# Performance work log

Measured on AMD Instinct MI355X. Metric: run time of the kernel, lower is better.

The kernel has to match this reference:

```python
import jax, jax.numpy as jnp
import numpy as np

CHUNK = 1000  # CHUNK_SIZE in the torch source
H = 8         # num_heads


def _depthwise_chunked(x_t, Wl, bl):
    """Replicates torch per-chunk local_conv (depthwise k=3, pad=1) + residual.
    Zero padding occurs at every chunk boundary, exactly as in the source loop.
    x_t: [B, C, L] with L divisible by CHUNK. Wl: [C,1,3], bl: [C].
    """
    B, C, L = x_t.shape
    n = L // CHUNK
    xc = x_t.reshape(B, C, n, CHUNK).transpose(0, 2, 1, 3).reshape(B * n, C, CHUNK)
    y = jax.lax.conv_general_dilated(
        xc, Wl, window_strides=(1,), padding=((1, 1),),
        feature_group_count=C, dimension_numbers=('NCH', 'OIH', 'NCH'))
    y = y + bl[None, :, None] + xc  # conv bias + residual (kv_chunk = local_conv(kv_chunk) + kv_chunk)
    return y.reshape(B, n, C, CHUNK).transpose(0, 2, 1, 3).reshape(B, C, L)


def setup_inputs() -> dict:
    key = jax.random.key(0)
    ks = jax.random.split(key, 8)
    B, L, C = 4, 2000, 512
    x = jax.random.normal(ks[0], (B, L, C), dtype=jnp.float32)
    rpe = jax.random.normal(ks[1], (1, H, L, L), dtype=jnp.float32) * 0.02
    s = 1.0 / np.sqrt(C)
    Wq = jax.random.normal(ks[2], (C, C), dtype=jnp.float32) * s      # q: Conv1d(dim,dim,1)
    bq = jnp.zeros((C,), dtype=jnp.float32)
    Wkv = jax.random.normal(ks[3], (2 * C, C), dtype=jnp.float32) * s # kv: Conv1d(dim,2dim,1)
    bkv = jnp.zeros((2 * C,), dtype=jnp.float32)
    Wl = jax.random.normal(ks[4], (C, 1, 3), dtype=jnp.float32) * (1.0 / np.sqrt(3.0))  # depthwise k=3
    bl = jnp.zeros((C,), dtype=jnp.float32)
    return {"x": x, "relative_pos_enc": rpe, "Wq": Wq, "bq": bq,
            "Wkv": Wkv, "bkv": bkv, "Wl": Wl, "bl": bl}


def reference(x, relative_pos_enc, Wq, bq, Wkv, bkv, Wl, bl):
    B, L, C = x.shape
    hd = C // H
    scale = hd ** (-0.5)
    x_t = jnp.swapaxes(x, 1, 2)  # [B, C, L]
    # q projection (1x1 conv == linear over channels)
    q = jnp.einsum('oc,bcl->bol', Wq, x_t) + bq[None, :, None]
    q = q.reshape(B, H, hd, L).transpose(0, 1, 3, 2)  # [B, H, L, hd]
    # K/V path: sr = Identity (sr_ratio=1); chunked depthwise local conv + residual
    kv_in = _depthwise_chunked(x_t, Wl, bl)           # [B, C, L]
    kv = jnp.einsum('oc,bcl->bol', Wkv, kv_in) + bkv[None, :, None]  # [B, 2C, L]
    k = kv[:, :C].reshape(B, H, hd, L)                # [B, H, hd, L]
    v = kv[:, C:].reshape(B, H, hd, L).transpose(0, 1, 3, 2)  # [B, H, L, hd]
    # attention with additive relative-position bias (chunking over rows in the
    # source is math-equivalent since softmax rows are independent)
    attn = jnp.einsum('bhld,bhdm->bhlm', q, k) * scale + relative_pos_enc
    attn = jax.nn.softmax(attn, axis=-1)
    out = jnp.einsum('bhlm,bhmd->bhld', attn, v)      # [B, H, L, hd]
    # source: cat -> [B,H,L,hd] -> transpose(-1,-2) -> [B,H,hd,L] -> reshape(B,L,C)
    return out.transpose(0, 1, 3, 2).reshape(B, L, C)
```

## Files before the change

### kernel.cpp

```cpp
#include <hip/hip_runtime.h>

#define B_ 4
#define L_ 2000
#define LP 2048
#define C_ 512
#define H_ 8
#define HD 64
#define CHUNK_ 1000

typedef __attribute__((ext_vector_type(8))) short bf16x8;
typedef __attribute__((ext_vector_type(4))) float f32x4;

__device__ inline unsigned short f2bf(float f) {
    union { float f; unsigned int u; } v; v.f = f;
    unsigned int r = v.u + 0x7fffu + ((v.u >> 16) & 1u);
    return (unsigned short)(r >> 16);
}

__global__ void conv_kernel(const float* __restrict__ x, const float* __restrict__ Wl,
                            const float* __restrict__ bl,
                            unsigned short* __restrict__ kv16,
                            unsigned short* __restrict__ x16) {
    int i4 = blockIdx.x * 256 + threadIdx.x;
    if (i4 >= B_ * L_ * C_ / 4) return;
    int idx = i4 * 4;
    int c = idx & (C_ - 1);
    int l = (idx >> 9) % L_;
    int p = l % CHUNK_;
    float4 xc = *(const float4*)&x[idx];
    float4 lf = (p > 0)          ? *(const float4*)&x[idx - C_] : make_float4(0, 0, 0, 0);
    float4 rt = (p < CHUNK_ - 1) ? *(const float4*)&x[idx + C_] : make_float4(0, 0, 0, 0);
    float y[4];
    const float* xcp = &xc.x; const float* lfp = &lf.x; const float* rtp = &rt.x;
#pragma unroll
    for (int j = 0; j < 4; j++) {
        y[j] = xcp[j] + bl[c + j] + Wl[(c + j) * 3 + 0] * lfp[j]
             + Wl[(c + j) * 3 + 1] * xcp[j] + Wl[(c + j) * 3 + 2] * rtp[j];
    }
    ushort4 kv = make_ushort4(f2bf(y[0]), f2bf(y[1]), f2bf(y[2]), f2bf(y[3]));
    ushort4 xo = make_ushort4(f2bf(xcp[0]), f2bf(xcp[1]), f2bf(xcp[2]), f2bf(xcp[3]));
    *(ushort4*)&kv16[idx] = kv;
    *(ushort4*)&x16[idx]  = xo;
}

__global__ void cvt_kernel(const float* __restrict__ Wq, const float* __restrict__ Wkv,
                           unsigned short* __restrict__ Wq16,
                           unsigned short* __restrict__ Wkv16) {
    int i4 = blockIdx.x * 256 + threadIdx.x;
    int idx = i4 * 4;
    const float* src; unsigned short* dst; int off;
    if (idx < 262144) { src = Wq; dst = Wq16; off = idx; }
    else if (idx < 786432) { src = Wkv; dst = Wkv16; off = idx - 262144; }
    else return;
    float4 v = *(const float4*)&src[off];
    *(ushort4*)&dst[off] = make_ushort4(f2bf(v.x), f2bf(v.y), f2bf(v.z), f2bf(v.w));
}

__global__ __launch_bounds__(256) void proj_mfma(
    const unsigned short* __restrict__ A, const unsigned short* __restrict__ W,
    const float* __restrict__ bias,
    unsigned short* __restrict__ o0, unsigned short* __restrict__ o1, int mode) {
    __shared__ __align__(16) unsigned short tile[64][72];
    const int tid = threadIdx.x;
    const int lane = tid & 63;
    const int wave = tid >> 6;
    const int c = lane & 15;
    const int quad = lane >> 4;
    const int mrow = blockIdx.x * 64 + wave * 16 + c;
    const int n0 = blockIdx.y * 64;
    f32x4 acc[4] = {{0,0,0,0},{0,0,0,0},{0,0,0,0},{0,0,0,0}};
    const unsigned short* Ap = A + (size_t)mrow * C_ + quad * 8;
#pragma unroll 4
    for (int k0 = 0; k0 < C_; k0 += 32) {
        bf16x8 a = *(const bf16x8*)(Ap + k0);
#pragma unroll
        for (int t = 0; t < 4; t++) {
            bf16x8 wv = *(const bf16x8*)&W[(size_t)(n0 + 16 * t + c) * C_ + k0 + quad * 8];
            acc[t] = __builtin_amdgcn_mfma_f32_16x16x32_bf16(a, wv, acc[t], 0, 0, 0);
        }
    }
    const bool vpath = (mode == 1 && n0 >= C_);
    const int lm = wave * 16 + quad * 4;
#pragma unroll
    for (int t = 0; t < 4; t++) {
        float bv = bias[n0 + 16 * t + c];
#pragma unroll
        for (int r = 0; r < 4; r++) {
            unsigned short val = f2bf(acc[t][r] + bv);
            if (!vpath) tile[lm + r][16 * t + c] = val;
            else        tile[16 * t + c][lm + r] = val;
        }
    }
    __syncthreads();
    if (!vpath) {
        int lr = tid >> 2, chunk = (tid & 3) * 16;
        int m = blockIdx.x * 64 + lr;
        int b = m / L_, l = m % L_;
        int nn = (n0 + chunk) & (C_ - 1);
        int h = nn >> 6, d0 = nn & 63;
        unsigned short* dst = &o0[(((size_t)(b * H_ + h) * LP) + l) * HD + d0];
        *(uint4*)dst       = *(const uint4*)&tile[lr][chunk];
        *(uint4*)(dst + 8) = *(const uint4*)&tile[lr][chunk + 8];
    } else {
        int dr = tid >> 2, chunk = (tid & 3) * 16;
        int nn = (n0 - C_) + dr;
        int h = nn >> 6, d = nn & 63;
        int mbase = blockIdx.x * 64 + chunk;
        int b0 = mbase / L_, b1 = (mbase + 15) / L_;
        if (b0 == b1) {
            int l = mbase % L_;
            unsigned short* dst = &o1[(((size_t)(b0 * H_ + h) * HD) + d) * LP + l];
            *(uint4*)dst       = *(const uint4*)&tile[dr][chunk];
            *(uint4*)(dst + 8) = *(const uint4*)&tile[dr][chunk + 8];
        } else {
            for (int i = 0; i < 16; i++) {
                int m = mbase + i;
                int b = m / L_, l = m % L_;
                o1[(((size_t)(b * H_ + h) * HD) + d) * LP + l] = tile[dr][chunk + i];
            }
        }
    }
}

__global__ __launch_bounds__(256, 2) void attn_mfma(
    const unsigned short* __restrict__ Q, const unsigned short* __restrict__ K,
    const unsigned short* __restrict__ Vt, const float* __restrict__ rpe,
    float* __restrict__ po, float* __restrict__ lsum) {
    __shared__ __align__(16) unsigned short Ks[4][32][72];
    __shared__ __align__(16) unsigned short Vs[4][64][40];
    __shared__ __align__(16) unsigned short Ps[4][2][16][40];
    const int tid = threadIdx.x;
    const int lane = tid & 63;
    const int wave = tid >> 6;
    const int c = lane & 15;
    const int quad = lane >> 4;
    const int bid = blockIdx.x;
    const int ks = bid & 1;
    const int h  = (bid >> 1) & 7;
    const int rt = bid >> 4;
    const int r0w = rt * 64 + wave * 16;
    const int rg0 = r0w + quad * 4;
    const int rgc = min(r0w + c, L_ - 1);
    const float* rrow = rpe + (size_t)h * L_ * L_ + (size_t)rgc * L_;

    const int krow = tid >> 3, kcol = (tid & 7) * 8;
    const int vrow = tid >> 2, vcol = (tid & 3) * 8;

    const int kt0 = ks * 32, kt1 = kt0 + 32;

    const unsigned short* Kb0 = K + (size_t)(0 * H_ + h) * LP * HD
        + (size_t)krow * HD + kcol + (size_t)(kt0 * 32) * HD;
    const unsigned short* Kb1 = Kb0 + (size_t)H_ * LP * HD;
    const unsigned short* Kb2 = Kb1 + (size_t)H_ * LP * HD;
    const unsigned short* Kb3 = Kb2 + (size_t)H_ * LP * HD;
    const unsigned short* Vb0 = Vt + (size_t)(0 * H_ + h) * HD * LP
        + (size_t)vrow * LP + vcol + kt0 * 32;
    const unsigned short* Vb1 = Vb0 + (size_t)H_ * HD * LP;
    const unsigned short* Vb2 = Vb1 + (size_t)H_ * HD * LP;
    const unsigned short* Vb3 = Vb2 + (size_t)H_ * HD * LP;

    bf16x8 qf0[4], qf1[4];
#pragma unroll
    for (int b = 0; b < 4; b++) {
        const unsigned short* Qb = Q + (size_t)(b * H_ + h) * LP * HD;
        qf0[b] = *(const bf16x8*)&Qb[(size_t)(r0w + c) * HD + quad * 8];
        qf1[b] = *(const bf16x8*)&Qb[(size_t)(r0w + c) * HD + 32 + quad * 8];
    }

    float l_i[4] = {0.f, 0.f, 0.f, 0.f};
    f32x4 o_acc[4][4];
#pragma unroll
    for (int b = 0; b < 4; b++)
#pragma unroll
        for (int t = 0; t < 4; t++) o_acc[b][t] = (f32x4){0.f, 0.f, 0.f, 0.f};

    const float LOG2E = 1.44269504f;
#define LOAD_RPE(d0, d1, KT)                                                 \
    {                                                                        \
        int cb0 = (KT) * 32 + quad * 4;                                      \
        int cb1 = cb0 + 16;                                                  \
        float4 raw0 = *(const float4*)&rrow[min(cb0, L_ - 4)];               \
        float4 raw1 = *(const float4*)&rrow[min(cb1, L_ - 4)];               \
        d0 = (cb0 <= L_ - 4) ? make_float4(raw0.x * LOG2E, raw0.y * LOG2E,   \
                                           raw0.z * LOG2E, raw0.w * LOG2E)  \
                             : make_float4(-1e30f, -1e30f, -1e30f, -1e30f);  \
        d1 = (cb1 <= L_ - 4) ? make_float4(raw1.x * LOG2E, raw1.y * LOG2E,   \
                                           raw1.z * LOG2E, raw1.w * LOG2E)  \
                             : make_float4(-1e30f, -1e30f, -1e30f, -1e30f);  \
    }

    uint4 kpre0 = *(const uint4*)Kb0, kpre1 = *(const uint4*)Kb1;
    uint4 kpre2 = *(const uint4*)Kb2, kpre3 = *(const uint4*)Kb3;
    uint4 vpre0 = *(const uint4*)Vb0, vpre1 = *(const uint4*)Vb1;
    uint4 vpre2 = *(const uint4*)Vb2, vpre3 = *(const uint4*)Vb3;
    float4 rpl0, rpl1;
    LOAD_RPE(rpl0, rpl1, kt0)

    for (int kt = kt0; kt < kt1; kt++) {
        __syncthreads();
        *(uint4*)&Ks[0][krow][kcol] = kpre0;
        *(uint4*)&Ks[1][krow][kcol] = kpre1;
        *(uint4*)&Ks[2][krow][kcol] = kpre2;
        *(uint4*)&Ks[3][krow][kcol] = kpre3;
        *(uint4*)&Vs[0][vrow][vcol] = vpre0;
        *(uint4*)&Vs[1][vrow][vcol] = vpre1;
        *(uint4*)&Vs[2][vrow][vcol] = vpre2;
        *(uint4*)&Vs[3][vrow][vcol] = vpre3;
        __syncthreads();

        float4 rpn0, rpn1;
        if (kt + 1 < kt1) {
            const size_t ko = (size_t)(kt + 1 - kt0) * 32 * HD;
            const int    vo = (kt + 1 - kt0) * 32;
            kpre0 = *(const uint4*)(Kb0 + ko);
            kpre1 = *(const uint4*)(Kb1 + ko);
            kpre2 = *(const uint4*)(Kb2 + ko);
            kpre3 = *(const uint4*)(Kb3 + ko);
            vpre0 = *(const uint4*)(Vb0 + vo);
            vpre1 = *(const uint4*)(Vb1 + vo);
            vpre2 = *(const uint4*)(Vb2 + vo);
            vpre3 = *(const uint4*)(Vb3 + vo);
            LOAD_RPE(rpn0, rpn1, kt + 1)
        }

#pragma unroll
        for (int b = 0; b < 4; b++) {
            f32x4 s0, s1;
            {
                bf16x8 k0f = *(const bf16x8*)&Ks[b][c][quad * 8];
                bf16x8 k1f = *(const bf16x8*)&Ks[b][c][32 + quad * 8];
                f32x4 z = {0.f, 0.f, 0.f, 0.f};
                z = __builtin_amdgcn_mfma_f32_16x16x32_bf16(k0f, qf0[b], z, 0, 0, 0);
                s0 = __builtin_amdgcn_mfma_f32_16x16x32_bf16(k1f, qf1[b], z, 0, 0, 0);
            }
            {
                bf16x8 k0f = *(const bf16x8*)&Ks[b][16 + c][quad * 8];
                bf16x8 k1f = *(const bf16x8*)&Ks[b][16 + c][32 + quad * 8];
                f32x4 z = {0.f, 0.f, 0.f, 0.f};
                z = __builtin_amdgcn_mfma_f32_16x16x32_bf16(k0f, qf0[b], z, 0, 0, 0);
                s1 = __builtin_amdgcn_mfma_f32_16x16x32_bf16(k1f, qf1[b], z, 0, 0, 0);
            }
            float psum;
            {
                float p0 = exp2f(fmaf(s0[0], 0.18033688f, rpl0.x));
                float p1 = exp2f(fmaf(s0[1], 0.18033688f, rpl0.y));
                float p2 = exp2f(fmaf(s0[2], 0.18033688f, rpl0.z));
                float p3 = exp2f(fmaf(s0[3], 0.18033688f, rpl0.w));
                psum = (p0 + p1) + (p2 + p3);
                *(ushort4*)&Ps[wave][b & 1][c][quad * 4] =
                    make_ushort4(f2bf(p0), f2bf(p1), f2bf(p2), f2bf(p3));
            }
            {
                float p0 = exp2f(fmaf(s1[0], 0.18033688f, rpl1.x));
                float p1 = exp2f(fmaf(s1[1], 0.18033688f, rpl1.y));
                float p2 = exp2f(fmaf(s1[2], 0.18033688f, rpl1.z));
                float p3 = exp2f(fmaf(s1[3], 0.18033688f, rpl1.w));
                psum += (p0 + p1) + (p2 + p3);
                *(ushort4*)&Ps[wave][b & 1][c][16 + quad * 4] =
                    make_ushort4(f2bf(p0), f2bf(p1), f2bf(p2), f2bf(p3));
            }
            l_i[b] += psum;
            bf16x8 pa = *(const bf16x8*)&Ps[wave][b & 1][c][quad * 8];
#pragma unroll
            for (int t = 0; t < 4; t++) {
                bf16x8 v0 = *(const bf16x8*)&Vs[b][16 * t + c][quad * 8];
                o_acc[b][t] = __builtin_amdgcn_mfma_f32_16x16x32_bf16(pa, v0, o_acc[b][t], 0, 0, 0);
            }
        }
        if (kt + 1 < kt1) { rpl0 = rpn0; rpl1 = rpn1; }
    }

#pragma unroll
    for (int b = 0; b < 4; b++) {
        float v = l_i[b];
        v += __shfl_xor(v, 16);
        v += __shfl_xor(v, 32);
        float* pob = po + (size_t)(ks * 32 + b * H_ + h) * L_ * HD;
#pragma unroll
        for (int t = 0; t < 4; t++) {
            int d = 16 * t + c;
#pragma unroll
            for (int r = 0; r < 4; r++) {
                int l = rg0 + r;
                if (l < L_) pob[(size_t)l * HD + d] = o_acc[b][t][r];
            }
        }
        if (lane < 16) {
            float* lb = lsum + (size_t)(ks * 32 + b * H_ + h) * LP;
            lb[r0w + lane] = v;
        }
    }
#undef LOAD_RPE
}

__global__ __launch_bounds__(256) void merge_kernel(
    const float* __restrict__ po, const float* __restrict__ lsum,
    float* __restrict__ out) {
    __shared__ __align__(16) float T[64][68];
    const int tid = threadIdx.x;
    const int bh = blockIdx.x >> 5;
    const int lt = blockIdx.x & 31;
    const float* p0 = po + (size_t)bh * L_ * HD;
    const float* p1 = p0 + (size_t)32 * L_ * HD;
    const float* ls0 = lsum + (size_t)bh * LP;
    const float* ls1 = ls0 + (size_t)32 * LP;
#pragma unroll
    for (int it = 0; it < 4; it++) {
        int idx = it * 256 + tid;
        int row = idx >> 4;
        int dc = (idx & 15) * 4;
        int l = lt * 64 + row;
        float4 v = make_float4(0.f, 0.f, 0.f, 0.f);
        if (l < L_) {
            float4 a  = *(const float4*)&p0[(size_t)l * HD + dc];
            float4 b4 = *(const float4*)&p1[(size_t)l * HD + dc];
            float inv = 1.f / (ls0[l] + ls1[l]);
            v = make_float4((a.x + b4.x) * inv, (a.y + b4.y) * inv,
                            (a.z + b4.z) * inv, (a.w + b4.w) * inv);
        }
        T[dc + 0][row] = v.x; T[dc + 1][row] = v.y;
        T[dc + 2][row] = v.z; T[dc + 3][row] = v.w;
    }
    __syncthreads();
    const int d = tid >> 2, ch = (tid & 3) * 16;
    const int lbase = lt * 64 + ch;
    if (lbase + 15 < L_) {
        float* dst = &out[((size_t)(bh * HD + d)) * L_ + lbase];
#pragma unroll
        for (int i = 0; i < 4; i++)
            *(float4*)&dst[4 * i] = *(const float4*)&T[d][ch + 4 * i];
    }
}

extern "C" void kernel_launch(void* const* d_in, const int* in_sizes, int n_in,
                              void* d_out, int out_size, void* d_ws, size_t ws_size,
                              hipStream_t stream) {
    const float* x   = (const float*)d_in[0];
    const float* rpe = (const float*)d_in[1];
    const float* Wq  = (const float*)d_in[2];
    const float* bq  = (const float*)d_in[3];
    const float* Wkv = (const float*)d_in[4];
    const float* bkv = (const float*)d_in[5];
    const float* Wl  = (const float*)d_in[6];
    const float* bl  = (const float*)d_in[7];
    float* out = (float*)d_out;

    unsigned short* wsu  = (unsigned short*)d_ws;
    unsigned short* x16  = wsu;
    unsigned short* kv16 = wsu + 4096000;
    unsigned short* Wq16 = wsu + 8192000;
    unsigned short* Wkv16= wsu + 8454144;
    unsigned short* Q16  = wsu + 8978432;
    unsigned short* K16  = wsu + 13172736;
    unsigned short* V16  = wsu + 17367040;
    float* po   = (float*)(wsu + 21561344);
    float* lsum = po + 8192000;

    conv_kernel<<<(B_ * L_ * C_ / 4 + 255) / 256, 256, 0, stream>>>(x, Wl, bl, kv16, x16);
    cvt_kernel<<<(786432 / 4 + 255) / 256, 256, 0, stream>>>(Wq, Wkv, Wq16, Wkv16);
    proj_mfma<<<dim3(125, 8), 256, 0, stream>>>(x16, Wq16, bq, Q16, nullptr, 0);
    proj_mfma<<<dim3(125, 16), 256, 0, stream>>>(kv16, Wkv16, bkv, K16, V16, 1);
    attn_mfma<<<512, 256, 0, stream>>>(Q16, K16, V16, rpe, po, lsum);
    merge_kernel<<<1024, 256, 0, stream>>>(po, lsum, out);
}
```

Measured before the change: 414.4 us.

## Split attention blocks across batch pairs to double grid and raise occupancy

Each attention block now handles two of the four batches instead of all four, so the grid doubles to 1024 blocks. This halves per-block registers, LDS and accumulators, and launch bounds are raised to allow 4 blocks per CU. The cost is that each rpe tile, which is shared across batches, is now read by two blocks instead of one, which doubles rpe global/L2 traffic.

```diff
diff --git a/kernel.cpp b/kernel.cpp
--- a/kernel.cpp
+++ b/kernel.cpp
@@ -122,12 +122,12 @@
     }
 }
 
-__global__ __launch_bounds__(256, 2) void attn_mfma(
+__global__ __launch_bounds__(256, 4) void attn_mfma(
     const unsigned short* __restrict__ Q, const unsigned short* __restrict__ K,
     const unsigned short* __restrict__ Vt, const float* __restrict__ rpe,
     float* __restrict__ po, float* __restrict__ lsum) {
-    __shared__ __align__(16) unsigned short Ks[4][32][72];
-    __shared__ __align__(16) unsigned short Vs[4][64][40];
+    __shared__ __align__(16) unsigned short Ks[2][32][72];
+    __shared__ __align__(16) unsigned short Vs[2][64][40];
     __shared__ __align__(16) unsigned short Ps[4][2][16][40];
     const int tid = threadIdx.x;
     const int lane = tid & 63;
@@ -137,7 +137,8 @@
     const int bid = blockIdx.x;
     const int ks = bid & 1;
     const int h  = (bid >> 1) & 7;
-    const int rt = bid >> 4;
+    const int bp = (bid >> 4) & 1;
+    const int rt = bid >> 5;
     const int r0w = rt * 64 + wave * 16;
     const int rg0 = r0w + quad * 4;
     const int rgc = min(r0w + c, L_ - 1);
@@ -148,29 +149,25 @@
 
     const int kt0 = ks * 32, kt1 = kt0 + 32;
 
-    const unsigned short* Kb0 = K + (size_t)(0 * H_ + h) * LP * HD
+    const unsigned short* Kb0 = K + (size_t)((bp * 2) * H_ + h) * LP * HD
         + (size_t)krow * HD + kcol + (size_t)(kt0 * 32) * HD;
     const unsigned short* Kb1 = Kb0 + (size_t)H_ * LP * HD;
-    const unsigned short* Kb2 = Kb1 + (size_t)H_ * LP * HD;
-    const unsigned short* Kb3 = Kb2 + (size_t)H_ * LP * HD;
-    const unsigned short* Vb0 = Vt + (size_t)(0 * H_ + h) * HD * LP
+    const unsigned short* Vb0 = Vt + (size_t)((bp * 2) * H_ + h) * HD * LP
         + (size_t)vrow * LP + vcol + kt0 * 32;
     const unsigned short* Vb1 = Vb0 + (size_t)H_ * HD * LP;
-    const unsigned short* Vb2 = Vb1 + (size_t)H_ * HD * LP;
-    const unsigned short* Vb3 = Vb2 + (size_t)H_ * HD * LP;
-
-    bf16x8 qf0[4], qf1[4];
-#pragma unroll
-    for (int b = 0; b < 4; b++) {
-        const unsigned short* Qb = Q + (size_t)(b * H_ + h) * LP * HD;
+
+    bf16x8 qf0[2], qf1[2];
+#pragma unroll
+    for (int b = 0; b < 2; b++) {
+        const unsigned short* Qb = Q + (size_t)((bp * 2 + b) * H_ + h) * LP * HD;
         qf0[b] = *(const bf16x8*)&Qb[(size_t)(r0w + c) * HD + quad * 8];
         qf1[b] = *(const bf16x8*)&Qb[(size_t)(r0w + c) * HD + 32 + quad * 8];
     }
 
-    float l_i[4] = {0.f, 0.f, 0.f, 0.f};
-    f32x4 o_acc[4][4];
-#pragma unroll
-    for (int b = 0; b < 4; b++)
+    float l_i[2] = {0.f, 0.f};
+    f32x4 o_acc[2][4];
+#pragma unroll
+    for (int b = 0; b < 2; b++)
 #pragma unroll
         for (int t = 0; t < 4; t++) o_acc[b][t] = (f32x4){0.f, 0.f, 0.f, 0.f};
 
@@ -190,9 +187,7 @@
     }
 
     uint4 kpre0 = *(const uint4*)Kb0, kpre1 = *(const uint4*)Kb1;
-    uint4 kpre2 = *(const uint4*)Kb2, kpre3 = *(const uint4*)Kb3;
     uint4 vpre0 = *(const uint4*)Vb0, vpre1 = *(const uint4*)Vb1;
-    uint4 vpre2 = *(const uint4*)Vb2, vpre3 = *(const uint4*)Vb3;
     float4 rpl0, rpl1;
     LOAD_RPE(rpl0, rpl1, kt0)
 
@@ -200,12 +195,8 @@
         __syncthreads();
         *(uint4*)&Ks[0][krow][kcol] = kpre0;
         *(uint4*)&Ks[1][krow][kcol] = kpre1;
-        *(uint4*)&Ks[2][krow][kcol] = kpre2;
-        *(uint4*)&Ks[3][krow][kcol] = kpre3;
         *(uint4*)&Vs[0][vrow][vcol] = vpre0;
         *(uint4*)&Vs[1][vrow][vcol] = vpre1;
-        *(uint4*)&Vs[2][vrow][vcol] = vpre2;
-        *(uint4*)&Vs[3][vrow][vcol] = vpre3;
         __syncthreads();
 
         float4 rpn0, rpn1;
@@ -214,17 +205,13 @@
             const int    vo = (kt + 1 - kt0) * 32;
             kpre0 = *(const uint4*)(Kb0 + ko);
             kpre1 = *(const uint4*)(Kb1 + ko);
-            kpre2 = *(const uint4*)(Kb2 + ko);
-            kpre3 = *(const uint4*)(Kb3 + ko);
             vpre0 = *(const uint4*)(Vb0 + vo);
             vpre1 = *(const uint4*)(Vb1 + vo);
-            vpre2 = *(const uint4*)(Vb2 + vo);
-            vpre3 = *(const uint4*)(Vb3 + vo);
             LOAD_RPE(rpn0, rpn1, kt + 1)
         }
 
 #pragma unroll
-        for (int b = 0; b < 4; b++) {
+        for (int b = 0; b < 2; b++) {
             f32x4 s0, s1;
             {
                 bf16x8 k0f = *(const bf16x8*)&Ks[b][c][quad * 8];
@@ -247,7 +234,7 @@
                 float p2 = exp2f(fmaf(s0[2], 0.18033688f, rpl0.z));
                 float p3 = exp2f(fmaf(s0[3], 0.18033688f, rpl0.w));
                 psum = (p0 + p1) + (p2 + p3);
-                *(ushort4*)&Ps[wave][b & 1][c][quad * 4] =
+                *(ushort4*)&Ps[wave][b][c][quad * 4] =
                     make_ushort4(f2bf(p0), f2bf(p1), f2bf(p2), f2bf(p3));
             }
             {
@@ -256,11 +243,11 @@
                 float p2 = exp2f(fmaf(s1[2], 0.18033688f, rpl1.z));
                 float p3 = exp2f(fmaf(s1[3], 0.18033688f, rpl1.w));
                 psum += (p0 + p1) + (p2 + p3);
-                *(ushort4*)&Ps[wave][b & 1][c][16 + quad * 4] =
+                *(ushort4*)&Ps[wave][b][c][16 + quad * 4] =
                     make_ushort4(f2bf(p0), f2bf(p1), f2bf(p2), f2bf(p3));
             }
             l_i[b] += psum;
-            bf16x8 pa = *(const bf16x8*)&Ps[wave][b & 1][c][quad * 8];
+            bf16x8 pa = *(const bf16x8*)&Ps[wave][b][c][quad * 8];
 #pragma unroll
             for (int t = 0; t < 4; t++) {
                 bf16x8 v0 = *(const bf16x8*)&Vs[b][16 * t + c][quad * 8];
@@ -271,11 +258,12 @@
     }
 
 #pragma unroll
-    for (int b = 0; b < 4; b++) {
+    for (int b = 0; b < 2; b++) {
+        const int rb = bp * 2 + b;
         float v = l_i[b];
         v += __shfl_xor(v, 16);
         v += __shfl_xor(v, 32);
-        float* pob = po + (size_t)(ks * 32 + b * H_ + h) * L_ * HD;
+        float* pob = po + (size_t)(ks * 32 + rb * H_ + h) * L_ * HD;
 #pragma unroll
         for (int t = 0; t < 4; t++) {
             int d = 16 * t + c;
@@ -286,7 +274,7 @@
             }
         }
         if (lane < 16) {
-            float* lb = lsum + (size_t)(ks * 32 + b * H_ + h) * LP;
+            float* lb = lsum + (size_t)(ks * 32 + rb * H_ + h) * LP;
             lb[r0w + lane] = v;
         }
     }
@@ -360,6 +348,6 @@
     cvt_kernel<<<(786432 / 4 + 255) / 256, 256, 0, stream>>>(Wq, Wkv, Wq16, Wkv16);
     proj_mfma<<<dim3(125, 8), 256, 0, stream>>>(x16, Wq16, bq, Q16, nullptr, 0);
     proj_mfma<<<dim3(125, 16), 256, 0, stream>>>(kv16, Wkv16, bkv, K16, V16, 1);
-    attn_mfma<<<512, 256, 0, stream>>>(Q16, K16, V16, rpe, po, lsum);
+    attn_mfma<<<1024, 256, 0, stream>>>(Q16, K16, V16, rpe, po, lsum);
     merge_kernel<<<1024, 256, 0, stream>>>(po, lsum, out);
 }
```

Result: no change. 410.9 us (-0.8%).
